# Performance work log

Measured on AMD Instinct MI355X. Metric: run time of the kernel, lower is better.

## Reference

```python
import jax, jax.numpy as jnp
import numpy as np

B, C_IN, IMG, P = 64, 3, 224, 16
L, H, E, NC = 12, 12, 768, 1000
HS = E // H          # 64
NSIDE = IMG // P     # 14
NP = NSIDE * NSIDE   # 196
T = NP + 1           # 197 tokens (cls + patches)
EPS = 1e-5


def setup_inputs() -> dict:
    key = jax.random.key(0)
    ks = jax.random.split(key, 16)
    s = 0.02
    inp = {}
    inp["x"] = jax.random.normal(ks[0], (B, C_IN, IMG, IMG), jnp.float32)
    # patch-embed conv (kernel=stride=P) as a linear on flattened patches
    inp["conv_w"] = jax.random.normal(ks[1], (E, C_IN, P, P), jnp.float32) * s
    inp["conv_b"] = jnp.zeros((E,), jnp.float32)
    inp["cls_token"] = jnp.zeros((1, 1, E), jnp.float32)
    inp["pos_embed"] = jax.random.normal(ks[2], (1, T, E), jnp.float32) * s
    # per-layer stacked params, stored in x @ W orientation
    inp["Wq"] = jax.random.normal(ks[3], (L, H, E, HS), jnp.float32) * s
    inp["Wk"] = jax.random.normal(ks[4], (L, H, E, HS), jnp.float32) * s
    inp["Wv"] = jax.random.normal(ks[5], (L, H, E, HS), jnp.float32) * s
    inp["proj_w"] = jax.random.normal(ks[6], (L, E, E), jnp.float32) * s
    inp["proj_b"] = jnp.zeros((L, E), jnp.float32)
    inp["ln1_g"] = jnp.ones((L, E), jnp.float32)
    inp["ln1_b"] = jnp.zeros((L, E), jnp.float32)
    inp["ln2_g"] = jnp.ones((L, E), jnp.float32)
    inp["ln2_b"] = jnp.zeros((L, E), jnp.float32)
    inp["ff1_w"] = jax.random.normal(ks[7], (L, E, 4 * E), jnp.float32) * s
    inp["ff1_b"] = jnp.zeros((L, 4 * E), jnp.float32)
    inp["ff2_w"] = jax.random.normal(ks[8], (L, 4 * E, E), jnp.float32) * s
    inp["ff2_b"] = jnp.zeros((L, E), jnp.float32)
    inp["lnf_g"] = jnp.ones((E,), jnp.float32)
    inp["lnf_b"] = jnp.zeros((E,), jnp.float32)
    inp["head_w"] = jax.random.normal(ks[9], (E, NC), jnp.float32) * s
    inp["head_b"] = jnp.zeros((NC,), jnp.float32)
    return inp


def _layernorm(x, g, b):
    m = x.mean(-1, keepdims=True)
    v = ((x - m) ** 2).mean(-1, keepdims=True)
    return (x - m) / jnp.sqrt(v + EPS) * g + b


def reference(x, conv_w, conv_b, cls_token, pos_embed, Wq, Wk, Wv, proj_w, proj_b,
              ln1_g, ln1_b, ln2_g, ln2_b, ff1_w, ff1_b, ff2_w, ff2_b,
              lnf_g, lnf_b, head_w, head_b):
    b = x.shape[0]
    # --- patch embedding: conv(k=s=P) == linear on flattened (c, ph, pw) patches ---
    xp = x.reshape(b, C_IN, NSIDE, P, NSIDE, P)
    xp = xp.transpose(0, 2, 4, 1, 3, 5).reshape(b, NP, C_IN * P * P)
    tok = xp @ conv_w.reshape(E, -1).T + conv_b  # [b, NP, E]
    cls = jnp.broadcast_to(cls_token, (b, 1, E))
    h = jnp.concatenate([cls, tok], axis=1) + pos_embed  # [b, T, E]

    for i in range(L):
        # --- MTG multi-head attention ---
        xn = _layernorm(h, ln1_g[i], ln1_b[i])
        q = jnp.einsum('btc,hcd->bhtd', xn, Wq[i])
        k = jnp.einsum('btc,hcd->bhtd', xn, Wk[i])
        v = jnp.einsum('btc,hcd->bhtd', xn, Wv[i])
        wei = jnp.einsum('bhtd,bhsd->bhts', q, k) * (HS ** -0.5)
        wei = wei - wei.mean(-1, keepdims=True)           # score centering
        var = (wei * wei).mean(-1, keepdims=True)          # population variance
        wei = jax.nn.softmax(wei / jnp.sqrt(var + EPS), axis=-1)
        attn_out = jnp.einsum('bhts,bhsd->bthd', wei, v).reshape(b, T, E)
        h = h + attn_out @ proj_w[i] + proj_b[i]
        # --- feed-forward ---
        xn2 = _layernorm(h, ln2_g[i], ln2_b[i])
        ff = jax.nn.gelu(xn2 @ ff1_w[i] + ff1_b[i], approximate=False)
        h = h + ff @ ff2_w[i] + ff2_b[i]

    h = _layernorm(h, lnf_g, lnf_b)
    logits = h[:, 0] @ head_w + head_b  # cls token head
    return logits
```

## Files before the change

### kernel.cpp

```cpp
#include <hip/hip_runtime.h>
#include <hip/hip_bf16.h>
#include <cstdint>
#include <cstddef>

typedef __bf16 bf16_t;
typedef __bf16 bf16x8 __attribute__((ext_vector_type(8)));
typedef __bf16 bf16x4 __attribute__((ext_vector_type(4)));
typedef float  f32x4  __attribute__((ext_vector_type(4)));

#define M_TOK 12608
#define M_PAD 12672
#define TPADV 224


__device__ __forceinline__ void gload_lds16(const void* g, void* lds) {
  __builtin_amdgcn_global_load_lds(
      (const __attribute__((address_space(1))) void*)g,
      (__attribute__((address_space(3))) void*)lds, 16, 0, 0);
}

__device__ __forceinline__ float wred64(float v) {
  v += __shfl_xor(v, 32); v += __shfl_xor(v, 16); v += __shfl_xor(v, 8);
  v += __shfl_xor(v, 4);  v += __shfl_xor(v, 2);  v += __shfl_xor(v, 1);
  return v;
}

__device__ __forceinline__ float rowred16(float v) {
  v += __shfl_xor(v, 1); v += __shfl_xor(v, 2);
  v += __shfl_xor(v, 4); v += __shfl_xor(v, 8);
  return v;
}

__device__ __forceinline__ float gelu_fast(float x) {
  const float z = fabsf(x) * 0.70710678118654752f;
  const float t = 1.f / (1.f + 0.3275911f * z);
  const float poly = t * (0.254829592f + t * (-0.284496736f + t * (1.421413741f +
                      t * (-1.453152027f + t * 1.061405429f))));
  const float erfz = 1.f - poly * __expf(-z * z);
  const float erfv = copysignf(erfz, x);
  return 0.5f * x * (1.f + erfv);
}


__global__ void tconv_kernel(const float* __restrict__ in, bf16_t* __restrict__ out,
                             int Kd, int Nd) {
  __shared__ float t[32][33];
  const float* ip = in + (size_t)blockIdx.z * Kd * Nd;
  bf16_t* op = out + (size_t)blockIdx.z * Kd * Nd;
  const int n0 = blockIdx.x * 32, k0 = blockIdx.y * 32;
  const int tx = threadIdx.x, ty = threadIdx.y;
#pragma unroll
  for (int r = 0; r < 32; r += 8)
    t[ty + r][tx] = ip[(size_t)(k0 + ty + r) * Nd + n0 + tx];
  __syncthreads();
#pragma unroll
  for (int r = 0; r < 32; r += 8)
    op[(size_t)(n0 + ty + r) * Kd + k0 + tx] = (bf16_t)t[tx][ty + r];
}

__global__ void qkvconv_kernel(const float* __restrict__ Wq, const float* __restrict__ Wk,
                               const float* __restrict__ Wv, bf16_t* __restrict__ out) {
  __shared__ float t[32][33];
  const int z = blockIdx.z;
  const int li = z / 36, rem = z % 36, which = rem / 12, hh = rem % 12;
  const float* W = (which == 0) ? Wq : ((which == 1) ? Wk : Wv);
  const float* ip = W + (size_t)(li * 12 + hh) * 768 * 64;
  bf16_t* op = out + (size_t)li * 2304 * 768 + (size_t)(which * 768 + hh * 64) * 768;
  const int k0 = blockIdx.x * 32, d0 = blockIdx.y * 32;
  const int tx = threadIdx.x, ty = threadIdx.y;
#pragma unroll
  for (int r = 0; r < 32; r += 8)
    t[ty + r][tx] = ip[(size_t)(k0 + ty + r) * 64 + d0 + tx];
  __syncthreads();
#pragma unroll
  for (int r = 0; r < 32; r += 8)
    op[(size_t)(d0 + ty + r) * 768 + k0 + tx] = (bf16_t)t[tx][ty + r];
}

__global__ void headwconv_kernel(const float* __restrict__ in, bf16_t* __restrict__ out) {
  __shared__ float t[32][33];
  const int n0 = blockIdx.x * 32, k0 = blockIdx.y * 32;
  const int tx = threadIdx.x, ty = threadIdx.y;
#pragma unroll
  for (int r = 0; r < 32; r += 8)
    t[ty + r][tx] = (n0 + tx < 1000) ? in[(size_t)(k0 + ty + r) * 1000 + n0 + tx] : 0.f;
  __syncthreads();
#pragma unroll
  for (int r = 0; r < 32; r += 8)
    out[(size_t)(n0 + ty + r) * 768 + k0 + tx] = (bf16_t)t[tx][ty + r];
}

__global__ void cast_kernel(const float* __restrict__ in, bf16_t* __restrict__ out, int n4) {
  const int id = blockIdx.x * 256 + threadIdx.x;
  if (id >= n4) return;
  float4 v = ((const float4*)in)[id];
  bf16x4 o;
  o[0] = (bf16_t)v.x; o[1] = (bf16_t)v.y; o[2] = (bf16_t)v.z; o[3] = (bf16_t)v.w;
  *(bf16x4*)(out + (size_t)id * 4) = o;
}

__global__ void zerovt_kernel(bf16_t* __restrict__ vtb, int n8) {
  bf16x8 z;
#pragma unroll
  for (int k = 0; k < 8; ++k) z[k] = (bf16_t)0.f;
  for (int id = blockIdx.x * 256 + threadIdx.x; id < n8; id += gridDim.x * 256)
    *(bf16x8*)(vtb + (size_t)id * 8) = z;
}


__global__ __launch_bounds__(256) void patch_kernel(const float* __restrict__ x,
                                                    bf16_t* __restrict__ xp) {
  const int id = blockIdx.x * 256 + threadIdx.x;
  const int m = id / 48, rem = id % 48;
  const int c = rem >> 4, iy = rem & 15;
  const int pb = m / 196, pp = m - pb * 196;
  const int py = pp / 14, px = pp - py * 14;
  const float4* src = (const float4*)(x + ((size_t)(pb * 3 + c) * 224 + py * 16 + iy) * 224 + px * 16);
  bf16_t* dst = xp + (size_t)m * 768 + c * 256 + iy * 16;
  float4 v0 = src[0], v1 = src[1], v2 = src[2], v3 = src[3];
  bf16x8 o0, o1;
  o0[0] = (bf16_t)v0.x; o0[1] = (bf16_t)v0.y; o0[2] = (bf16_t)v0.z; o0[3] = (bf16_t)v0.w;
  o0[4] = (bf16_t)v1.x; o0[5] = (bf16_t)v1.y; o0[6] = (bf16_t)v1.z; o0[7] = (bf16_t)v1.w;
  o1[0] = (bf16_t)v2.x; o1[1] = (bf16_t)v2.y; o1[2] = (bf16_t)v2.z; o1[3] = (bf16_t)v2.w;
  o1[4] = (bf16_t)v3.x; o1[5] = (bf16_t)v3.y; o1[6] = (bf16_t)v3.z; o1[7] = (bf16_t)v3.w;
  *(bf16x8*)dst = o0;
  *(bf16x8*)(dst + 8) = o1;
}

__global__ void cls_kernel(const float* __restrict__ cls, const float* __restrict__ pos,
                           float* __restrict__ h) {
  const int b = blockIdx.x;
  for (int e = threadIdx.x; e < 768; e += 256)
    h[(size_t)b * 197 * 768 + e] = cls[e] + pos[e];
}

__global__ __launch_bounds__(256) void ln_kernel(const float* __restrict__ h,
    const float* __restrict__ g, const float* __restrict__ bb,
    bf16_t* __restrict__ out, int rows) {
  const int wv = threadIdx.x >> 6, ln = threadIdx.x & 63;
  const int row = blockIdx.x * 4 + wv;
  if (row >= rows) return;
  const float4* hp = (const float4*)(h + (size_t)row * 768);
  float4 xv[3];
  xv[0] = hp[ln]; xv[1] = hp[ln + 64]; xv[2] = hp[ln + 128];
  float s = 0.f;
#pragma unroll
  for (int k = 0; k < 3; ++k) s += xv[k].x + xv[k].y + xv[k].z + xv[k].w;
  s = wred64(s);
  const float mean = s * (1.f / 768.f);
  float vs = 0.f;
#pragma unroll
  for (int k = 0; k < 3; ++k) {
    float a = xv[k].x - mean, b2 = xv[k].y - mean, c = xv[k].z - mean, d = xv[k].w - mean;
    vs += a * a + b2 * b2 + c * c + d * d;
  }
  vs = wred64(vs);
  const float rstd = rsqrtf(vs * (1.f / 768.f) + 1e-5f);
  const float4* gp = (const float4*)g;
  const float4* bp = (const float4*)bb;
  bf16_t* op = out + (size_t)row * 768;
#pragma unroll
  for (int k = 0; k < 3; ++k) {
    const int i4 = ln + 64 * k;
    const float4 gv = gp[i4], bv = bp[i4];
    bf16x4 o;
    o[0] = (bf16_t)((xv[k].x - mean) * rstd * gv.x + bv.x);
    o[1] = (bf16_t)((xv[k].y - mean) * rstd * gv.y + bv.y);
    o[2] = (bf16_t)((xv[k].z - mean) * rstd * gv.z + bv.z);
    o[3] = (bf16_t)((xv[k].w - mean) * rstd * gv.w + bv.w);
    *(bf16x4*)(op + i4 * 4) = o;
  }
}

__global__ __launch_bounds__(256) void lnf_cls_kernel(const float* __restrict__ h,
    const float* __restrict__ g, const float* __restrict__ bb, bf16_t* __restrict__ out) {
  const int wv = threadIdx.x >> 6, ln = threadIdx.x & 63;
  const int b = blockIdx.x * 4 + wv;
  bf16_t* op = out + (size_t)b * 768;
  if (b >= 64) {
    bf16x4 z; z[0] = z[1] = z[2] = z[3] = (bf16_t)0.f;
#pragma unroll
    for (int k = 0; k < 3; ++k) *(bf16x4*)(op + (ln + 64 * k) * 4) = z;
    return;
  }
  const float4* hp = (const float4*)(h + (size_t)b * 197 * 768);
  float4 xv[3];
  xv[0] = hp[ln]; xv[1] = hp[ln + 64]; xv[2] = hp[ln + 128];
  float s = 0.f;
#pragma unroll
  for (int k = 0; k < 3; ++k) s += xv[k].x + xv[k].y + xv[k].z + xv[k].w;
  s = wred64(s);
  const float mean = s * (1.f / 768.f);
  float vs = 0.f;
#pragma unroll
  for (int k = 0; k < 3; ++k) {
    float a = xv[k].x - mean, b2 = xv[k].y - mean, c = xv[k].z - mean, d = xv[k].w - mean;
    vs += a * a + b2 * b2 + c * c + d * d;
  }
  vs = wred64(vs);
  const float rstd = rsqrtf(vs * (1.f / 768.f) + 1e-5f);
  const float4* gp = (const float4*)g;
  const float4* bp = (const float4*)bb;
#pragma unroll
  for (int k = 0; k < 3; ++k) {
    const int i4 = ln + 64 * k;
    const float4 gv = gp[i4], bv = bp[i4];
    bf16x4 o;
    o[0] = (bf16_t)((xv[k].x - mean) * rstd * gv.x + bv.x);
    o[1] = (bf16_t)((xv[k].y - mean) * rstd * gv.y + bv.y);
    o[2] = (bf16_t)((xv[k].z - mean) * rstd * gv.z + bv.z);
    o[3] = (bf16_t)((xv[k].w - mean) * rstd * gv.w + bv.w);
    *(bf16x4*)(op + i4 * 4) = o;
  }
}


enum { EPI_PATCH = 0, EPI_QKV = 1, EPI_BIAS_RES = 2, EPI_GELU = 3, EPI_HEAD = 4 };

template <int EPI>
__global__ __launch_bounds__(256, 4)
void gemm128(const bf16_t* __restrict__ A, const bf16_t* __restrict__ Bt,
             int Mvalid, int K, int NT,
             void* __restrict__ out0, const float* __restrict__ bias,
             const float* __restrict__ pos, bf16_t* __restrict__ vtbuf, int ldo) {
  __shared__ __align__(16) bf16_t LdsAll[2][2][128 * 32];

  const int nwg = gridDim.x;
  const int orig = blockIdx.x;
  const int q8 = nwg >> 3, r8 = nwg & 7;
  const int xcd = orig & 7, idx8 = orig >> 3;
  const int wgid = (xcd < r8 ? xcd * (q8 + 1) : r8 * (q8 + 1) + (xcd - r8) * q8) + idx8;
  const int mt = wgid / NT, nt = wgid - mt * NT;

  const int tid = threadIdx.x;
  const int wv = tid >> 6, ln = tid & 63;
  const int wm = wv >> 1, wn = wv & 1;
  const int tl = ln & 15, kg = ln >> 4;
  const int KT = K >> 5;

  const int lr = ln >> 2, lq = ln & 3;
  const int la0 = wv * 32 + lr, la1 = wv * 32 + 16 + lr;
  const int ga0 = lq ^ ((la0 >> 1) & 3), ga1 = lq ^ ((la1 >> 1) & 3);
  const bf16_t* pA0 = A + (size_t)(mt * 128 + la0) * K + ga0 * 8;
  const bf16_t* pA1 = A + (size_t)(mt * 128 + la1) * K + ga1 * 8;
  const bf16_t* pB0 = Bt + (size_t)(nt * 128 + la0) * K + ga0 * 8;
  const bf16_t* pB1 = Bt + (size_t)(nt * 128 + la1) * K + ga1 * 8;
  const int c0 = wv * 1024, c1 = wv * 1024 + 512;

#define STAGE(b_, kt_)                                               \
  { gload_lds16(pA0 + (size_t)(kt_) * 32, &LdsAll[0][b_][c0]);       \
    gload_lds16(pA1 + (size_t)(kt_) * 32, &LdsAll[0][b_][c1]);       \
    gload_lds16(pB0 + (size_t)(kt_) * 32, &LdsAll[1][b_][c0]);       \
    gload_lds16(pB1 + (size_t)(kt_) * 32, &LdsAll[1][b_][c1]); }

  f32x4 acc[4][4];
#pragma unroll
  for (int i = 0; i < 4; ++i)
#pragma unroll
    for (int j = 0; j < 4; ++j) {
      acc[i][j][0] = 0.f; acc[i][j][1] = 0.f; acc[i][j][2] = 0.f; acc[i][j][3] = 0.f;
    }

  STAGE(0, 0);
  __syncthreads();
  for (int kt = 0; kt < KT; ++kt) {
    const int buf = kt & 1;
    if (kt + 1 < KT) STAGE(buf ^ 1, kt + 1);
    bf16x8 af[4], bfr[4];
#pragma unroll
    for (int i = 0; i < 4; ++i) {
      const int ra = wm * 64 + i * 16 + tl;
      af[i] = *(const bf16x8*)(((const char*)&LdsAll[0][buf][0]) + ra * 64 +
                               (((kg ^ (ra >> 1)) & 3) << 4));
    }
#pragma unroll
    for (int j = 0; j < 4; ++j) {
      const int rb = wn * 64 + j * 16 + tl;
      bfr[j] = *(const bf16x8*)(((const char*)&LdsAll[1][buf][0]) + rb * 64 +
                                (((kg ^ (rb >> 1)) & 3) << 4));
    }
    __builtin_amdgcn_s_setprio(1);
#pragma unroll
    for (int i = 0; i < 4; ++i)
#pragma unroll
      for (int j = 0; j < 4; ++j)
        acc[i][j] = __builtin_amdgcn_mfma_f32_16x16x32_bf16(af[i], bfr[j], acc[i][j], 0, 0, 0);
    __builtin_amdgcn_s_setprio(0);
    __syncthreads();
  }
#undef STAGE

  const int mb = mt * 128 + wm * 64, nb = nt * 128 + wn * 64;

  if constexpr (EPI == EPI_QKV) {
    if (nt >= 12) {
      char* Tl = (char*)&LdsAll[0][0][0];
      const int dblk = nt * 128 - 1536;
#pragma unroll
      for (int i = 0; i < 4; ++i)
#pragma unroll
        for (int j = 0; j < 4; ++j)
#pragma unroll
          for (int r = 0; r < 4; ++r) {
            const int m_l = wm * 64 + i * 16 + kg * 4 + r;
            const int d_l = wn * 64 + j * 16 + tl;
            const int quad = (d_l >> 3) ^ (m_l & 15) ^ ((m_l >> 4) & 3);
            *(bf16_t*)(Tl + m_l * 256 + quad * 16 + (d_l & 7) * 2) = (bf16_t)acc[i][j][r];
          }
      __syncthreads();
      const int mB = mt * 128;
#pragma unroll
      for (int e4 = 0; e4 < 64; ++e4) {
        const int e = e4 * 256 + tid;
        const int m_l = e & 127, d_l = e >> 7;
        const int m = mB + m_l;
        if (m < Mvalid) {
          const int quad = (d_l >> 3) ^ (m_l & 15) ^ ((m_l >> 4) & 3);
          const bf16_t val = *(const bf16_t*)(Tl + m_l * 256 + quad * 16 + (d_l & 7) * 2);
          const int dv = dblk + d_l;
          const int pb = m / 197, tt = m - pb * 197;
          vtbuf[((size_t)(pb * 12 + (dv >> 6)) * 64 + (dv & 63)) * TPADV + tt] = val;
        }
      }
      return;
    }
  }

#pragma unroll
  for (int i = 0; i < 4; ++i) {
#pragma unroll
    for (int j = 0; j < 4; ++j) {
#pragma unroll
      for (int r = 0; r < 4; ++r) {
        const int m = mb + i * 16 + kg * 4 + r;
        const int n = nb + j * 16 + tl;
        if (m >= Mvalid) continue;
        const float v = acc[i][j][r];
        if constexpr (EPI == EPI_PATCH) {
          const int pb = m / 196, pp = m - pb * 196;
          const float val = v + bias[n] + pos[(size_t)(pp + 1) * 768 + n];
          ((float*)out0)[(size_t)(m + pb + 1) * 768 + n] = val;
        } else if constexpr (EPI == EPI_QKV) {
          ((bf16_t*)out0)[(size_t)m * 1536 + n] = (bf16_t)v;
        } else if constexpr (EPI == EPI_BIAS_RES) {
          float* hp = (float*)out0 + (size_t)m * 768 + n;
          *hp += v + bias[n];
        } else if constexpr (EPI == EPI_HEAD) {
          if (n < 1000)
            ((float*)out0)[(size_t)m * 1000 + n] = v + bias[n];
        } else {
          ((bf16_t*)out0)[(size_t)m * (size_t)ldo + n] = (bf16_t)gelu_fast(v + bias[n]);
        }
      }
    }
  }
}

__global__ __launch_bounds__(256, 2)
void attn_kernel(const bf16_t* __restrict__ qk, const bf16_t* __restrict__ vt,
                 bf16_t* __restrict__ attno) {
  __shared__ bf16_t Kl[224 * 72];
  __shared__ bf16_t Pl[4][16 * 232];
  const int bh = blockIdx.x;
  const int b = bh / 12, hh = bh % 12;
  const int tid = threadIdx.x, wv = tid >> 6, ln = tid & 63;
  const int tl = ln & 15, kg = ln >> 4;

  for (int idx = tid; idx < 224 * 8; idx += 256) {
    const int s = idx >> 3, c = idx & 7;
    bf16x8 val;
    if (s < 197) {
      val = *(const bf16x8*)(qk + (size_t)(b * 197 + s) * 1536 + 768 + hh * 64 + c * 8);
    } else {
#pragma unroll
      for (int j2 = 0; j2 < 8; ++j2) val[j2] = (bf16_t)0.f;
    }
    *(bf16x8*)&Kl[s * 72 + c * 8] = val;
  }
  __syncthreads();

  for (int qt = wv; qt < 13; qt += 4) {
    const size_t qoff = (size_t)(b * 197 + qt * 16 + tl) * 1536 + hh * 64 + kg * 8;
    const bf16x8 aq0 = *(const bf16x8*)(qk + qoff);
    const bf16x8 aq1 = *(const bf16x8*)(qk + qoff + 32);
    f32x4 sc[13];
#pragma unroll
    for (int st = 0; st < 13; ++st) {
      const bf16x8 bk0 = *(const bf16x8*)&Kl[(st * 16 + tl) * 72 + kg * 8];
      const bf16x8 bk1 = *(const bf16x8*)&Kl[(st * 16 + tl) * 72 + 32 + kg * 8];
      f32x4 z = {0.f, 0.f, 0.f, 0.f};
      z = __builtin_amdgcn_mfma_f32_16x16x32_bf16(aq0, bk0, z, 0, 0, 0);
      z = __builtin_amdgcn_mfma_f32_16x16x32_bf16(aq1, bk1, z, 0, 0, 0);
      sc[st] = z;
    }
#pragma unroll
    for (int st = 0; st < 13; ++st)
#pragma unroll
      for (int r = 0; r < 4; ++r) sc[st][r] *= 0.125f;

    float inv[4];
#pragma unroll
    for (int r = 0; r < 4; ++r) {
      float sum = 0.f;
#pragma unroll
      for (int st = 0; st < 13; ++st)
        if (st * 16 + tl < 197) sum += sc[st][r];
      sum = rowred16(sum);
      const float mean = sum * (1.f / 197.f);
      float ss = 0.f;
#pragma unroll
      for (int st = 0; st < 13; ++st)
        if (st * 16 + tl < 197) { const float cc = sc[st][r] - mean; ss += cc * cc; }
      ss = rowred16(ss);
      const float rstd = rsqrtf(ss * (1.f / 197.f) + 1e-5f);
      float ps = 0.f;
#pragma unroll
      for (int st = 0; st < 13; ++st) {
        const int s = st * 16 + tl;
        float p = 0.f;
        if (s < 197) p = __expf((sc[st][r] - mean) * rstd);
        ps += p;
        Pl[wv][(kg * 4 + r) * 232 + st * 16 + tl] = (bf16_t)p;
      }
      ps = rowred16(ps);
      inv[r] = 1.f / ps;
      Pl[wv][(kg * 4 + r) * 232 + 208 + tl] = (bf16_t)0.f;
      if (tl < 8) Pl[wv][(kg * 4 + r) * 232 + 224 + tl] = (bf16_t)0.f;
    }

    f32x4 oa[4];
#pragma unroll
    for (int nf = 0; nf < 4; ++nf) {
      oa[nf][0] = 0.f; oa[nf][1] = 0.f; oa[nf][2] = 0.f; oa[nf][3] = 0.f;
    }
#pragma unroll
    for (int kk = 0; kk < 7; ++kk) {
      const bf16x8 pa = *(const bf16x8*)&Pl[wv][tl * 232 + kk * 32 + kg * 8];
#pragma unroll
      for (int nf = 0; nf < 4; ++nf) {
        const bf16x8 vb = *(const bf16x8*)(vt + ((size_t)bh * 64 + nf * 16 + tl) * TPADV + kk * 32 + kg * 8);
        oa[nf] = __builtin_amdgcn_mfma_f32_16x16x32_bf16(pa, vb, oa[nf], 0, 0, 0);
      }
    }
#pragma unroll
    for (int nf = 0; nf < 4; ++nf)
#pragma unroll
      for (int r = 0; r < 4; ++r) {
        const int t = qt * 16 + kg * 4 + r;
        if (t < 197)
          attno[(size_t)(b * 197 + t) * 768 + hh * 64 + nf * 16 + tl] =
              (bf16_t)(oa[nf][r] * inv[r]);
      }
  }
}


extern "C" void kernel_launch(void* const* d_in, const int* in_sizes, int n_in,
                              void* d_out, int out_size, void* d_ws, size_t ws_size,
                              hipStream_t stream) {
  (void)in_sizes; (void)n_in; (void)out_size; (void)ws_size;
  const float* x      = (const float*)d_in[0];
  const float* conv_w = (const float*)d_in[1];
  const float* conv_b = (const float*)d_in[2];
  const float* cls_t  = (const float*)d_in[3];
  const float* pos    = (const float*)d_in[4];
  const float* Wq     = (const float*)d_in[5];
  const float* Wk     = (const float*)d_in[6];
  const float* Wv     = (const float*)d_in[7];
  const float* proj_w = (const float*)d_in[8];
  const float* proj_b = (const float*)d_in[9];
  const float* ln1_g  = (const float*)d_in[10];
  const float* ln1_b  = (const float*)d_in[11];
  const float* ln2_g  = (const float*)d_in[12];
  const float* ln2_b  = (const float*)d_in[13];
  const float* ff1_w  = (const float*)d_in[14];
  const float* ff1_b  = (const float*)d_in[15];
  const float* ff2_w  = (const float*)d_in[16];
  const float* ff2_b  = (const float*)d_in[17];
  const float* lnf_g  = (const float*)d_in[18];
  const float* lnf_b  = (const float*)d_in[19];
  const float* head_w = (const float*)d_in[20];
  const float* head_b = (const float*)d_in[21];
  float* out = (float*)d_out;

  char* w = (char*)d_ws;
  size_t off = 0;
  auto take = [&](size_t bytes) {
    char* p = w + off;
    off = (off + bytes + 255) & ~(size_t)255;
    return p;
  };
  bf16_t* Wc_t    = (bf16_t*)take((size_t)768 * 768 * 2);
  bf16_t* Wqkv_t  = (bf16_t*)take((size_t)12 * 2304 * 768 * 2);
  bf16_t* Wproj_t = (bf16_t*)take((size_t)12 * 768 * 768 * 2);
  bf16_t* Wff1_t  = (bf16_t*)take((size_t)12 * 3072 * 768 * 2);
  bf16_t* Wff2_t  = (bf16_t*)take((size_t)12 * 768 * 3072 * 2);
  bf16_t* Wht     = (bf16_t*)take((size_t)1024 * 768 * 2);
  float*  hbuf    = (float*)take((size_t)M_PAD * 768 * 4);
  bf16_t* xn      = (bf16_t*)take((size_t)M_PAD * 768 * 2);
  bf16_t* qkb     = (bf16_t*)take((size_t)M_PAD * 1536 * 2);
  bf16_t* vtb     = (bf16_t*)take((size_t)768 * 64 * TPADV * 2);
  bf16_t* attno   = (bf16_t*)take((size_t)M_PAD * 768 * 2);
  bf16_t* ffa     = (bf16_t*)take((size_t)M_PAD * 3072 * 2);
  bf16_t* xcls    = (bf16_t*)take((size_t)256 * 768 * 2);

  const dim3 blk256(256);
  const dim3 tb(32, 8);

  tconv_kernel<<<dim3(24, 24, 12), tb, 0, stream>>>(proj_w, Wproj_t, 768, 768);
  tconv_kernel<<<dim3(96, 24, 12), tb, 0, stream>>>(ff1_w, Wff1_t, 768, 3072);
  tconv_kernel<<<dim3(24, 96, 12), tb, 0, stream>>>(ff2_w, Wff2_t, 3072, 768);
  qkvconv_kernel<<<dim3(24, 2, 432), tb, 0, stream>>>(Wq, Wk, Wv, Wqkv_t);
  headwconv_kernel<<<dim3(32, 24), tb, 0, stream>>>(head_w, Wht);
  cast_kernel<<<dim3(576), blk256, 0, stream>>>(conv_w, Wc_t, 147456);
  zerovt_kernel<<<dim3(2048), blk256, 0, stream>>>(vtb, 768 * 64 * TPADV / 8);

  patch_kernel<<<dim3(2352), blk256, 0, stream>>>(x, xn);
  cls_kernel<<<dim3(64), blk256, 0, stream>>>(cls_t, pos, hbuf);
  gemm128<EPI_PATCH><<<dim3(6 * 98), blk256, 0, stream>>>(
      xn, Wc_t, 12544, 768, 6, (void*)hbuf, conv_b, pos, (bf16_t*)nullptr, 768);

  for (int i = 0; i < 12; ++i) {
    ln_kernel<<<dim3(3152), blk256, 0, stream>>>(hbuf, ln1_g + i * 768, ln1_b + i * 768, xn, M_TOK);
    gemm128<EPI_QKV><<<dim3(18 * 99), blk256, 0, stream>>>(
        xn, Wqkv_t + (size_t)i * 2304 * 768, M_TOK, 768, 18, (void*)qkb,
        (const float*)nullptr, (const float*)nullptr, vtb, 1536);
    attn_kernel<<<dim3(768), blk256, 0, stream>>>(qkb, vtb, attno);
    gemm128<EPI_BIAS_RES><<<dim3(6 * 99), blk256, 0, stream>>>(
        attno, Wproj_t + (size_t)i * 768 * 768, M_TOK, 768, 6, (void*)hbuf,
        proj_b + i * 768, (const float*)nullptr, (bf16_t*)nullptr, 768);
    ln_kernel<<<dim3(3152), blk256, 0, stream>>>(hbuf, ln2_g + i * 768, ln2_b + i * 768, xn, M_TOK);
    gemm128<EPI_GELU><<<dim3(24 * 99), blk256, 0, stream>>>(
        xn, Wff1_t + (size_t)i * 768 * 3072, M_TOK, 768, 24, (void*)ffa,
        ff1_b + i * 3072, (const float*)nullptr, (bf16_t*)nullptr, 3072);
    gemm128<EPI_BIAS_RES><<<dim3(6 * 99), blk256, 0, stream>>>(
        ffa, Wff2_t + (size_t)i * 3072 * 768, M_TOK, 3072, 6, (void*)hbuf,
        ff2_b + i * 768, (const float*)nullptr, (bf16_t*)nullptr, 768);
  }

  lnf_cls_kernel<<<dim3(64), blk256, 0, stream>>>(hbuf, lnf_g, lnf_b, xcls);
  gemm128<EPI_HEAD><<<dim3(16), blk256, 0, stream>>>(
      xcls, Wht, 64, 768, 8, (void*)out, head_b, (const float*)nullptr,
      (bf16_t*)nullptr, 1000);
}
```

Measured before the change: 4.674 ms.

## Enlarge GEMM tile to 256x128 with 512-thread workgroups

```diff
diff --git a/kernel.cpp b/kernel.cpp
--- a/kernel.cpp
+++ b/kernel.cpp
@@ -9,7 +9,7 @@
 typedef float  f32x4  __attribute__((ext_vector_type(4)));
 
 #define M_TOK 12608
-#define M_PAD 12672
+#define M_PAD 12800
 #define TPADV 224
 
 
@@ -218,12 +218,13 @@
 enum { EPI_PATCH = 0, EPI_QKV = 1, EPI_BIAS_RES = 2, EPI_GELU = 3, EPI_HEAD = 4 };
 
 template <int EPI>
-__global__ __launch_bounds__(256, 4)
-void gemm128(const bf16_t* __restrict__ A, const bf16_t* __restrict__ Bt,
+__global__ __launch_bounds__(512, 4)
+void gemm256(const bf16_t* __restrict__ A, const bf16_t* __restrict__ Bt,
              int Mvalid, int K, int NT,
              void* __restrict__ out0, const float* __restrict__ bias,
              const float* __restrict__ pos, bf16_t* __restrict__ vtbuf, int ldo) {
-  __shared__ __align__(16) bf16_t LdsAll[2][2][128 * 32];
+  __shared__ __align__(16) bf16_t Al[2][256 * 32];
+  __shared__ __align__(16) bf16_t Bl[2][128 * 32];
 
   const int nwg = gridDim.x;
   const int orig = blockIdx.x;
@@ -239,19 +240,20 @@
   const int KT = K >> 5;
 
   const int lr = ln >> 2, lq = ln & 3;
-  const int la0 = wv * 32 + lr, la1 = wv * 32 + 16 + lr;
+  const int la0 = wv * 32 + lr, la1 = la0 + 16;
+  const int lb0 = wv * 16 + lr;
   const int ga0 = lq ^ ((la0 >> 1) & 3), ga1 = lq ^ ((la1 >> 1) & 3);
-  const bf16_t* pA0 = A + (size_t)(mt * 128 + la0) * K + ga0 * 8;
-  const bf16_t* pA1 = A + (size_t)(mt * 128 + la1) * K + ga1 * 8;
-  const bf16_t* pB0 = Bt + (size_t)(nt * 128 + la0) * K + ga0 * 8;
-  const bf16_t* pB1 = Bt + (size_t)(nt * 128 + la1) * K + ga1 * 8;
-  const int c0 = wv * 1024, c1 = wv * 1024 + 512;
-
-#define STAGE(b_, kt_)                                               \
-  { gload_lds16(pA0 + (size_t)(kt_) * 32, &LdsAll[0][b_][c0]);       \
-    gload_lds16(pA1 + (size_t)(kt_) * 32, &LdsAll[0][b_][c1]);       \
-    gload_lds16(pB0 + (size_t)(kt_) * 32, &LdsAll[1][b_][c0]);       \
-    gload_lds16(pB1 + (size_t)(kt_) * 32, &LdsAll[1][b_][c1]); }
+  const int gb0 = lq ^ ((lb0 >> 1) & 3);
+  const bf16_t* pA0 = A + (size_t)(mt * 256 + la0) * K + ga0 * 8;
+  const bf16_t* pA1 = A + (size_t)(mt * 256 + la1) * K + ga1 * 8;
+  const bf16_t* pB0 = Bt + (size_t)(nt * 128 + lb0) * K + gb0 * 8;
+  const int cA0 = wv * 1024, cA1 = cA0 + 512;
+  const int cB0 = wv * 512;
+
+#define STAGE(b_, kt_)                                          \
+  { gload_lds16(pA0 + (size_t)(kt_) * 32, &Al[b_][cA0]);        \
+    gload_lds16(pA1 + (size_t)(kt_) * 32, &Al[b_][cA1]);        \
+    gload_lds16(pB0 + (size_t)(kt_) * 32, &Bl[b_][cB0]); }
 
   f32x4 acc[4][4];
 #pragma unroll
@@ -270,13 +272,13 @@
 #pragma unroll
     for (int i = 0; i < 4; ++i) {
       const int ra = wm * 64 + i * 16 + tl;
-      af[i] = *(const bf16x8*)(((const char*)&LdsAll[0][buf][0]) + ra * 64 +
+      af[i] = *(const bf16x8*)(((const char*)&Al[buf][0]) + ra * 64 +
                                (((kg ^ (ra >> 1)) & 3) << 4));
     }
 #pragma unroll
     for (int j = 0; j < 4; ++j) {
       const int rb = wn * 64 + j * 16 + tl;
-      bfr[j] = *(const bf16x8*)(((const char*)&LdsAll[1][buf][0]) + rb * 64 +
+      bfr[j] = *(const bf16x8*)(((const char*)&Bl[buf][0]) + rb * 64 +
                                 (((kg ^ (rb >> 1)) & 3) << 4));
     }
     __builtin_amdgcn_s_setprio(1);
@@ -290,37 +292,43 @@
   }
 #undef STAGE
 
-  const int mb = mt * 128 + wm * 64, nb = nt * 128 + wn * 64;
+  const int mb = mt * 256 + wm * 64, nb = nt * 128 + wn * 64;
 
   if constexpr (EPI == EPI_QKV) {
     if (nt >= 12) {
-      char* Tl = (char*)&LdsAll[0][0][0];
+      char* Tl = (char*)&Al[0][0];
       const int dblk = nt * 128 - 1536;
 #pragma unroll
-      for (int i = 0; i < 4; ++i)
-#pragma unroll
-        for (int j = 0; j < 4; ++j)
-#pragma unroll
-          for (int r = 0; r < 4; ++r) {
-            const int m_l = wm * 64 + i * 16 + kg * 4 + r;
-            const int d_l = wn * 64 + j * 16 + tl;
+      for (int h = 0; h < 2; ++h) {
+        if ((wm >> 1) == h) {
+#pragma unroll
+          for (int i = 0; i < 4; ++i)
+#pragma unroll
+            for (int j = 0; j < 4; ++j)
+#pragma unroll
+              for (int r = 0; r < 4; ++r) {
+                const int m_l = (wm & 1) * 64 + i * 16 + kg * 4 + r;
+                const int d_l = wn * 64 + j * 16 + tl;
+                const int quad = (d_l >> 3) ^ (m_l & 15) ^ ((m_l >> 4) & 3);
+                *(bf16_t*)(Tl + m_l * 256 + quad * 16 + (d_l & 7) * 2) =
+                    (bf16_t)acc[i][j][r];
+              }
+        }
+        __syncthreads();
+#pragma unroll
+        for (int e4 = 0; e4 < 32; ++e4) {
+          const int e = e4 * 512 + tid;
+          const int m_l = e & 127, d_l = e >> 7;
+          const int m = mt * 256 + h * 128 + m_l;
+          if (m < Mvalid) {
             const int quad = (d_l >> 3) ^ (m_l & 15) ^ ((m_l >> 4) & 3);
-            *(bf16_t*)(Tl + m_l * 256 + quad * 16 + (d_l & 7) * 2) = (bf16_t)acc[i][j][r];
+            const bf16_t val = *(const bf16_t*)(Tl + m_l * 256 + quad * 16 + (d_l & 7) * 2);
+            const int dv = dblk + d_l;
+            const int pb = m / 197, tt = m - pb * 197;
+            vtbuf[((size_t)(pb * 12 + (dv >> 6)) * 64 + (dv & 63)) * TPADV + tt] = val;
           }
-      __syncthreads();
-      const int mB = mt * 128;
-#pragma unroll
-      for (int e4 = 0; e4 < 64; ++e4) {
-        const int e = e4 * 256 + tid;
-        const int m_l = e & 127, d_l = e >> 7;
-        const int m = mB + m_l;
-        if (m < Mvalid) {
-          const int quad = (d_l >> 3) ^ (m_l & 15) ^ ((m_l >> 4) & 3);
-          const bf16_t val = *(const bf16_t*)(Tl + m_l * 256 + quad * 16 + (d_l & 7) * 2);
-          const int dv = dblk + d_l;
-          const int pb = m / 197, tt = m - pb * 197;
-          vtbuf[((size_t)(pb * 12 + (dv >> 6)) * 64 + (dv & 63)) * TPADV + tt] = val;
         }
+        __syncthreads();
       }
       return;
     }
@@ -505,6 +513,7 @@
   bf16_t* xcls    = (bf16_t*)take((size_t)256 * 768 * 2);
 
   const dim3 blk256(256);
+  const dim3 blk512(512);
   const dim3 tb(32, 8);
 
   tconv_kernel<<<dim3(24, 24, 12), tb, 0, stream>>>(proj_w, Wproj_t, 768, 768);
@@ -517,29 +526,29 @@
 
   patch_kernel<<<dim3(2352), blk256, 0, stream>>>(x, xn);
   cls_kernel<<<dim3(64), blk256, 0, stream>>>(cls_t, pos, hbuf);
-  gemm128<EPI_PATCH><<<dim3(6 * 98), blk256, 0, stream>>>(
+  gemm256<EPI_PATCH><<<dim3(49 * 6), blk512, 0, stream>>>(
       xn, Wc_t, 12544, 768, 6, (void*)hbuf, conv_b, pos, (bf16_t*)nullptr, 768);
 
   for (int i = 0; i < 12; ++i) {
     ln_kernel<<<dim3(3152), blk256, 0, stream>>>(hbuf, ln1_g + i * 768, ln1_b + i * 768, xn, M_TOK);
-    gemm128<EPI_QKV><<<dim3(18 * 99), blk256, 0, stream>>>(
+    gemm256<EPI_QKV><<<dim3(50 * 18), blk512, 0, stream>>>(
         xn, Wqkv_t + (size_t)i * 2304 * 768, M_TOK, 768, 18, (void*)qkb,
         (const float*)nullptr, (const float*)nullptr, vtb, 1536);
     attn_kernel<<<dim3(768), blk256, 0, stream>>>(qkb, vtb, attno);
-    gemm128<EPI_BIAS_RES><<<dim3(6 * 99), blk256, 0, stream>>>(
+    gemm256<EPI_BIAS_RES><<<dim3(50 * 6), blk512, 0, stream>>>(
         attno, Wproj_t + (size_t)i * 768 * 768, M_TOK, 768, 6, (void*)hbuf,
         proj_b + i * 768, (const float*)nullptr, (bf16_t*)nullptr, 768);
     ln_kernel<<<dim3(3152), blk256, 0, stream>>>(hbuf, ln2_g + i * 768, ln2_b + i * 768, xn, M_TOK);
-    gemm128<EPI_GELU><<<dim3(24 * 99), blk256, 0, stream>>>(
+    gemm256<EPI_GELU><<<dim3(50 * 24), blk512, 0, stream>>>(
         xn, Wff1_t + (size_t)i * 768 * 3072, M_TOK, 768, 24, (void*)ffa,
         ff1_b + i * 3072, (const float*)nullptr, (bf16_t*)nullptr, 3072);
-    gemm128<EPI_BIAS_RES><<<dim3(6 * 99), blk256, 0, stream>>>(
+    gemm256<EPI_BIAS_RES><<<dim3(50 * 6), blk512, 0, stream>>>(
         ffa, Wff2_t + (size_t)i * 3072 * 768, M_TOK, 3072, 6, (void*)hbuf,
         ff2_b + i * 768, (const float*)nullptr, (bf16_t*)nullptr, 768);
   }
 
   lnf_cls_kernel<<<dim3(64), blk256, 0, stream>>>(hbuf, lnf_g, lnf_b, xcls);
-  gemm128<EPI_HEAD><<<dim3(16), blk256, 0, stream>>>(
+  gemm256<EPI_HEAD><<<dim3(8), blk512, 0, stream>>>(
       xcls, Wht, 64, 768, 8, (void*)out, head_b, (const float*)nullptr,
       (bf16_t*)nullptr, 1000);
 }
```

After: 4.861 ms. +4.0%, slower.
